# Kernel optimization log

Hardware: AMD Instinct MI355X
Metric: run time of the kernel (lower is better)

Reference implementation:

```python
import jax, jax.numpy as jnp
import numpy as np
import math

# ---- hyperparameters (from __init__) ----
S = 64.0
M = 0.45
EASY_MARGIN = False
ALPHA = 0.0
BETA = 0.0
EPS_OT = 0.1   # self.eps
NITER = 6      # self.niter
COS_M = math.cos(M)
SIN_M = math.sin(M)
TH = math.cos(math.pi - M)
MM = math.sin(math.pi - M) * M

# ---- shapes ----
B = 24
D_EMB = 512
N_CLASSES = 10000
C_CH = 256   # channels -> number of OT points per image
H = 14       # spatial -> point dim H*H = 196


def setup_inputs() -> dict:
    key = jax.random.key(0)
    k1, k2, k3, k4 = jax.random.split(key, 4)
    embeddings = jax.random.normal(k1, (B, D_EMB), dtype=jnp.float32)
    conv_features = jax.random.normal(k2, (B, C_CH, H, H), dtype=jnp.float32)
    label = jax.random.randint(k3, (B,), 0, 8)
    # nn.init.normal_(kernel, std=0.01)
    kernel = jax.random.normal(k4, (D_EMB, N_CLASSES), dtype=jnp.float32) * 0.01
    return {"embeddings": embeddings, "conv_features": conv_features,
            "kernel": kernel, "label": label, "epoch": 1}


def _cdist(x, y):
    # Euclidean pairwise distance via GEMM: x (n,d), y (m,d) -> (n,m)
    x2 = jnp.sum(x * x, axis=-1)[:, None]
    y2 = jnp.sum(y * y, axis=-1)[None, :]
    d2 = jnp.maximum(x2 + y2 - 2.0 * (x @ y.T), 0.0)
    return jnp.sqrt(d2 + 1e-12)


def _sinkhorn_dist(x, y):
    # Entropic OT distance <T, C> with uniform marginals, log-domain Sinkhorn.
    C = _cdist(x, y)                       # (n, m)
    n, m = C.shape
    log_mu = -jnp.log(jnp.float32(n))
    log_nu = -jnp.log(jnp.float32(m))
    f = jnp.zeros((n,), C.dtype)
    g = jnp.zeros((m,), C.dtype)
    for _ in range(NITER):  # fixed 6 iterations
        f = -EPS_OT * jax.nn.logsumexp((g[None, :] - C) / EPS_OT + log_nu, axis=1)
        g = -EPS_OT * jax.nn.logsumexp((f[:, None] - C) / EPS_OT + log_mu, axis=0)
    T = jnp.exp((f[:, None] + g[None, :] - C) / EPS_OT + log_mu + log_nu)
    return jnp.sum(T * C)


def reference(embeddings, conv_features, kernel, label, epoch):
    b = embeddings.shape[0]
    emb = embeddings / jnp.linalg.norm(embeddings, axis=1, keepdims=True)
    kn = kernel / jnp.linalg.norm(kernel, axis=0, keepdims=True)
    cos_theta = jnp.clip(emb @ kn, -1.0, 1.0)          # (B, n_classes)
    origin_cos = cos_theta

    rows = jnp.arange(b)
    tl = cos_theta[rows, label]                         # target logit (B,)
    sin_t = jnp.sqrt(jnp.maximum(1.0 - tl * tl, 0.0))
    ctm = tl * COS_M - sin_t * SIN_M
    if EASY_MARGIN:
        ftl = jnp.where(tl > 0.0, ctm, tl)
    else:
        ftl = jnp.where(tl > TH, ctm, tl - MM)
    cos_theta = cos_theta.at[rows, label].set(ftl)
    arcfaceloss = cos_theta * S

    # ---- triplet mining on embedding cosine similarities ----
    dists = emb @ emb.T                                 # (B, B) cosine sims
    eq = label[:, None] == label[None, :]               # (B, B) same-class mask
    # diff_low[a,p,n] = cos(a,n) - cos(a,p)
    diff = dists[:, None, :] - dists[:, :, None]        # (a, p, n)
    valid = eq[:, :, None] & (~eq)[:, None, :] & (diff > -ALPHA)
    n_cosine_pair = jnp.sum(valid)

    if epoch >= 0:
        feats = conv_features.reshape(b, conv_features.shape[1], -1)  # (B, C, H*H)
        # batched Sinkhorn distance for all (a,b) image pairs: (B, B)
        D = jax.vmap(lambda xa: jax.vmap(lambda xb: _sinkhorn_dist(xa, xb))(feats))(feats)
        dis = jnp.maximum(D[:, :, None] - D[:, None, :], -BETA)       # (a, p, n)
        hit = valid & (dis > 0.0)
        ot_pair = jnp.sum(hit)
        wass = jnp.sum(jnp.where(hit, dis, 0.0))
        wass_loss = jnp.where(wass > 0.0,
                              wass / jnp.maximum(ot_pair, 1).astype(wass.dtype),
                              jnp.zeros((), wass.dtype))
    else:
        ot_pair = jnp.zeros((), jnp.int32)
        wass_loss = jnp.zeros(())

    return (arcfaceloss, wass_loss, origin_cos * S, n_cosine_pair, ot_pair)
```

## Files before the change

kernel.cpp:

```cpp
#include <hip/hip_runtime.h>
#include <math.h>

#define B_SZ 24
#define D_EMBD 512
#define N_CLS 10000
#define CC 256
#define HH 196

#define S_SCALE 64.0f
#define COS_M 0.9004471023526769f
#define SIN_M 0.43496553411123023f
#define TH_C (-0.9004471023526769f)
#define MM_C 0.19573449035005357f
#define KSC 14.4269504088896f
#define C2E 0.0693147180559945f

typedef short bfrag8 __attribute__((ext_vector_type(8)));
typedef float facc4 __attribute__((ext_vector_type(4)));

#if __has_builtin(__builtin_amdgcn_exp2f)
#define EXP2F(x) __builtin_amdgcn_exp2f(x)
#else
#define EXP2F(x) exp2f(x)
#endif
#if __has_builtin(__builtin_amdgcn_logf)
#define LOG2F(x) __builtin_amdgcn_logf(x)
#else
#define LOG2F(x) __log2f(x)
#endif

__device__ inline unsigned short f2bf_rne(float x) {
    union { float f; unsigned u; } cv; cv.f = x;
    unsigned r = cv.u + 0x7FFFu + ((cv.u >> 16) & 1u);
    return (unsigned short)(r >> 16);
}
__device__ inline float bf2f(unsigned short h) {
    union { unsigned u; float f; } cv; cv.u = ((unsigned)h) << 16; return cv.f;
}

__global__ __launch_bounds__(1024) void k_pairs_all(const float* __restrict__ emb,
        const float* __restrict__ conv, float* __restrict__ dists,
        float* __restrict__ Dmat) {
    const int t = threadIdx.x;
    const int bid = blockIdx.x;

    if (bid >= 276) {
        int l = t & 63, w16 = t >> 6;
        if (bid == 276 && t < B_SZ) Dmat[t * B_SZ + t] = 0.f;
        int pid = (bid - 276) * 16 + w16;
        if (pid >= B_SZ * B_SZ) return;
        int i = pid / B_SZ, j = pid - (pid / B_SZ) * B_SZ;
        float sij = 0.f, sii = 0.f, sjj = 0.f;
        #pragma unroll
        for (int u = 0; u < 8; ++u) {
            float vi = emb[i*D_EMBD + u*64 + l];
            float vj = emb[j*D_EMBD + u*64 + l];
            sij = fmaf(vi, vj, sij); sii = fmaf(vi, vi, sii); sjj = fmaf(vj, vj, sjj);
        }
        #pragma unroll
        for (int o = 1; o < 64; o <<= 1) {
            sij += __shfl_xor(sij, o, 64);
            sii += __shfl_xor(sii, o, 64);
            sjj += __shfl_xor(sjj, o, 64);
        }
        if (l == 0) dists[pid] = sij * rsqrtf(sii * sjj);
        return;
    }

    __shared__ __align__(16) char smem[65536];
    unsigned short* Ah = (unsigned short*)smem;
    unsigned short* Al = Ah + 8192;
    unsigned short* Bh = Al + 8192;
    unsigned short* Bl = Bh + 8192;
    float* rowred = (float*)smem;
    float* colred = rowred + 1024;
    float* rm_l   = colred + 1024;
    float* z_l    = rm_l + 256;
    float* g_l    = z_l + 256;
    float* na_s   = g_l + 256;
    float* nb_s   = na_s + 256;
    float* wredF  = nb_s + 256;
    float* wredG  = wredF + 4;
    float* wredD  = wredG + 4;

    const int w = t >> 6;
    const int wr = w >> 2, wc = w & 3;
    const int q = (t >> 4) & 3, c0 = t & 15;
    const int R0 = wr * 64, C0 = wc * 64;

    int rem = bid, a = 0;
    while (rem >= 23 - a) { rem -= 23 - a; ++a; }
    int b = a + 1 + rem;
    const float* xa = conv + a*CC*HH;
    const float* xb = conv + b*CC*HH;

    const int sn = t >> 2;
    const int sch = t & 3;

    facc4 acc[4][4];
    #pragma unroll
    for (int i = 0; i < 4; ++i)
        #pragma unroll
        for (int j = 0; j < 4; ++j) acc[i][j] = (facc4){0.f, 0.f, 0.f, 0.f};

    float pa = 0.f, pb = 0.f;

    for (int ks = 0; ks < 224; ks += 32) {
        __syncthreads();
        #pragma unroll
        for (int p = 0; p < 2; ++p) {
            int k0 = ks + sch*8;
            const float* src = (p ? xb : xa) + sn*HH + k0;
            float v[8];
            if (k0 + 8 <= HH) {
                const float4* s4 = (const float4*)src;
                float4 u0 = s4[0], u1 = s4[1];
                v[0]=u0.x; v[1]=u0.y; v[2]=u0.z; v[3]=u0.w;
                v[4]=u1.x; v[5]=u1.y; v[6]=u1.z; v[7]=u1.w;
            } else {
                #pragma unroll
                for (int j = 0; j < 8; ++j) v[j] = (k0 + j < HH) ? src[j] : 0.f;
            }
            float ps = 0.f;
            union { unsigned short s[8]; bfrag8 v8; } uh, ul;
            #pragma unroll
            for (int j = 0; j < 8; ++j) {
                ps = fmaf(v[j], v[j], ps);
                unsigned short hb = f2bf_rne(v[j]);
                uh.s[j] = hb;
                ul.s[j] = f2bf_rne(v[j] - bf2f(hb));
            }
            if (p) pb += ps; else pa += ps;
            unsigned short* dh = (p ? Bh : Ah) + sn*32 + sch*8;
            unsigned short* dl = (p ? Bl : Al) + sn*32 + sch*8;
            *(bfrag8*)dh = uh.v8;
            *(bfrag8*)dl = ul.v8;
        }
        __syncthreads();
        bfrag8 bh4[4], bl4[4];
        #pragma unroll
        for (int tj = 0; tj < 4; ++tj) {
            int col = C0 + tj*16 + c0;
            bh4[tj] = *(const bfrag8*)(Bh + col*32 + q*8);
            bl4[tj] = *(const bfrag8*)(Bl + col*32 + q*8);
        }
        #pragma unroll
        for (int ti = 0; ti < 4; ++ti) {
            int row = R0 + ti*16 + c0;
            bfrag8 ah = *(const bfrag8*)(Ah + row*32 + q*8);
            bfrag8 al = *(const bfrag8*)(Al + row*32 + q*8);
            #pragma unroll
            for (int tj = 0; tj < 4; ++tj) {
                acc[ti][tj] = __builtin_amdgcn_mfma_f32_16x16x32_bf16(ah, bh4[tj], acc[ti][tj], 0, 0, 0);
                acc[ti][tj] = __builtin_amdgcn_mfma_f32_16x16x32_bf16(ah, bl4[tj], acc[ti][tj], 0, 0, 0);
                acc[ti][tj] = __builtin_amdgcn_mfma_f32_16x16x32_bf16(al, bh4[tj], acc[ti][tj], 0, 0, 0);
            }
        }
    }
    __syncthreads();

    pa += __shfl_xor(pa, 1, 64); pa += __shfl_xor(pa, 2, 64);
    pb += __shfl_xor(pb, 1, 64); pb += __shfl_xor(pb, 2, 64);
    if (sch == 0) { na_s[sn] = pa; nb_s[sn] = pb; }
    if (t < 256) g_l[t] = 0.f;
    if (t < 4) wredG[t] = 0.f;
    __syncthreads();

    facc4 E[4][4];
    {
        float nbv[4];
        #pragma unroll
        for (int tj = 0; tj < 4; ++tj) nbv[tj] = nb_s[C0 + tj*16 + c0];
        #pragma unroll
        for (int ti = 0; ti < 4; ++ti) {
            facc4 nav = *(const facc4*)&na_s[R0 + ti*16 + q*4];
            #pragma unroll
            for (int tj = 0; tj < 4; ++tj) {
                #pragma unroll
                for (int r = 0; r < 4; ++r) {
                    float d2 = fmaxf(nav[r] + nbv[tj] - 2.f*acc[ti][tj][r], 0.f);
                    E[ti][tj][r] = KSC * sqrtf(d2 + 1e-12f);
                }
            }
        }
    }

    const int istar = ((c0&1)<<3) | ((c0&2)<<1) | ((c0&4)>>1) | ((c0&8)>>3);
    const int rowstar = R0 + (istar>>2)*16 + q*4 + (istar&3);
    const int tjstar = ((q&1)<<1) | (q>>1);
    const int colstar = C0 + tjstar*16 + c0;

    {
        float v16[16];
        #pragma unroll
        for (int ti = 0; ti < 4; ++ti)
            #pragma unroll
            for (int r = 0; r < 4; ++r)
                v16[ti*4+r] = fminf(fminf(E[ti][0][r], E[ti][1][r]),
                                    fminf(E[ti][2][r], E[ti][3][r]));
        #pragma unroll
        for (int p = 0; p < 4; ++p) {
            const int m = 1 << p, hsz = 8 >> p;
            const bool hi = (c0 >> p) & 1;
            #pragma unroll
            for (int j = 0; j < hsz; ++j) {
                float mine = hi ? v16[j+hsz] : v16[j];
                float send = hi ? v16[j] : v16[j+hsz];
                v16[j] = fminf(mine, __shfl_xor(send, m, 64));
            }
        }
        rowred[wc*256 + rowstar] = v16[0];
    }
    __syncthreads();
    if (t < 256)
        rm_l[t] = fminf(fminf(rowred[t], rowred[256+t]), fminf(rowred[512+t], rowred[768+t]));
    __syncthreads();

    #pragma unroll
    for (int ti = 0; ti < 4; ++ti) {
        facc4 rmv = *(const facc4*)&rm_l[R0 + ti*16 + q*4];
        #pragma unroll
        for (int tj = 0; tj < 4; ++tj)
            #pragma unroll
            for (int r = 0; r < 4; ++r)
                E[ti][tj][r] = EXP2F(rmv[r] - E[ti][tj][r]);
    }

    #pragma unroll 1
    for (int it = 0; it < 6; ++it) {
        float Gmax = fmaxf(fmaxf(wredG[0], wredG[1]), fmaxf(wredG[2], wredG[3]));
        float P4[4];
        #pragma unroll
        for (int tj = 0; tj < 4; ++tj) P4[tj] = EXP2F(g_l[C0 + tj*16 + c0] - Gmax);
        float v16[16];
        #pragma unroll
        for (int ti = 0; ti < 4; ++ti)
            #pragma unroll
            for (int r = 0; r < 4; ++r) {
                float s = 0.f;
                #pragma unroll
                for (int tj = 0; tj < 4; ++tj) s = fmaf(E[ti][tj][r], P4[tj], s);
                v16[ti*4+r] = s;
            }
        #pragma unroll
        for (int p = 0; p < 4; ++p) {
            const int m = 1 << p, hsz = 8 >> p;
            const bool hi = (c0 >> p) & 1;
            #pragma unroll
            for (int j = 0; j < hsz; ++j) {
                float mine = hi ? v16[j+hsz] : v16[j];
                float send = hi ? v16[j] : v16[j+hsz];
                v16[j] = mine + __shfl_xor(send, m, 64);
            }
        }
        rowred[wc*256 + rowstar] = v16[0];
        __syncthreads();
        if (t < 256) {
            float s = rowred[t] + rowred[256+t] + rowred[512+t] + rowred[768+t];
            float z = 8.f - Gmax - LOG2F(s);
            z_l[t] = z;
            float m = z;
            #pragma unroll
            for (int o = 1; o < 64; o <<= 1) m = fmaxf(m, __shfl_xor(m, o, 64));
            if ((t & 63) == 0) wredF[t >> 6] = m;
        }
        __syncthreads();
        float M = fmaxf(fmaxf(wredF[0], wredF[1]), fmaxf(wredF[2], wredF[3]));
        float Q[16];
        #pragma unroll
        for (int ti = 0; ti < 4; ++ti) {
            facc4 zv = *(const facc4*)&z_l[R0 + ti*16 + q*4];
            #pragma unroll
            for (int r = 0; r < 4; ++r) Q[ti*4+r] = EXP2F(zv[r] - M);
        }
        float w4[4];
        #pragma unroll
        for (int tj = 0; tj < 4; ++tj) {
            float s = 0.f;
            #pragma unroll
            for (int ti = 0; ti < 4; ++ti)
                #pragma unroll
                for (int r = 0; r < 4; ++r) s = fmaf(E[ti][tj][r], Q[ti*4+r], s);
            w4[tj] = s;
        }
        #pragma unroll
        for (int p = 0; p < 2; ++p) {
            const int m = 16 << p, hsz = 2 >> p;
            const bool hi = (q >> p) & 1;
            #pragma unroll
            for (int j = 0; j < hsz; ++j) {
                float mine = hi ? w4[j+hsz] : w4[j];
                float send = hi ? w4[j] : w4[j+hsz];
                w4[j] = mine + __shfl_xor(send, m, 64);
            }
        }
        colred[wr*256 + colstar] = w4[0];
        __syncthreads();
        if (t < 256) {
            float s = colred[t] + colred[256+t] + colred[512+t] + colred[768+t];
            float G = 8.f - M - LOG2F(s);
            g_l[t] = G;
            float m = G;
            #pragma unroll
            for (int o = 1; o < 64; o <<= 1) m = fmaxf(m, __shfl_xor(m, o, 64));
            if ((t & 63) == 0) wredG[t >> 6] = m;
        }
        __syncthreads();
    }

    {
        float G4[4];
        #pragma unroll
        for (int tj = 0; tj < 4; ++tj) G4[tj] = g_l[C0 + tj*16 + c0] - 16.f;
        float d = 0.f;
        #pragma unroll
        for (int ti = 0; ti < 4; ++ti) {
            facc4 zv = *(const facc4*)&z_l[R0 + ti*16 + q*4];
            facc4 rmv = *(const facc4*)&rm_l[R0 + ti*16 + q*4];
            #pragma unroll
            for (int tj = 0; tj < 4; ++tj) {
                #pragma unroll
                for (int r = 0; r < 4; ++r) {
                    float e = fmaxf(E[ti][tj][r], 1e-45f);
                    float lE = LOG2F(e);
                    float ce = rmv[r] - lE;
                    d = fmaf(EXP2F(zv[r] + G4[tj] + lE), ce, d);
                }
            }
        }
        d *= C2E;
        #pragma unroll
        for (int o = 1; o < 64; o <<= 1) d += __shfl_xor(d, o, 64);
        if ((t & 63) == 0) wredD[w] = d;
        __syncthreads();
        if (t == 0) {
            float s = 0.f;
            #pragma unroll
            for (int i = 0; i < 16; ++i) s += wredD[i];
            Dmat[a*B_SZ + b] = s;
            Dmat[b*B_SZ + a] = s;
        }
    }
}

__global__ __launch_bounds__(256) void k_arc_fin(const float* __restrict__ emb,
        const float* __restrict__ kern, const int* __restrict__ label,
        const float* __restrict__ dists, const float* __restrict__ Dmat,
        float* __restrict__ out) {
    const int t = threadIdx.x;
    const int bid = blockIdx.x;

    if (bid == 313) {
        __shared__ float ds[576], Dm[576];
        __shared__ int lab[B_SZ];
        __shared__ float wls[4]; __shared__ int wnp[4], wot[4];
        for (int i = t; i < 576; i += 256) { ds[i] = dists[i]; Dm[i] = Dmat[i]; }
        if (t < B_SZ) lab[t] = label[t];
        __syncthreads();
        int np = 0, ot = 0; float wsum = 0.f;
        for (int idx = t; idx < 24*24*24; idx += 256) {
            int a2 = idx / 576;
            int rest = idx - a2*576;
            int p2 = rest / 24;
            int n2 = rest - p2*24;
            int la = lab[a2];
            if (la == lab[p2] && la != lab[n2]) {
                float diff = ds[a2*24 + n2] - ds[a2*24 + p2];
                if (diff > 0.f) {
                    ++np;
                    float dd = Dm[a2*24 + p2] - Dm[a2*24 + n2];
                    if (dd > 0.f) { ++ot; wsum += dd; }
                }
            }
        }
        #pragma unroll
        for (int o = 1; o < 64; o <<= 1) {
            np += __shfl_xor(np, o, 64);
            ot += __shfl_xor(ot, o, 64);
            wsum += __shfl_xor(wsum, o, 64);
        }
        int w = t >> 6;
        if ((t & 63) == 0) { wnp[w] = np; wot[w] = ot; wls[w] = wsum; }
        __syncthreads();
        if (t == 0) {
            int tnp = wnp[0]+wnp[1]+wnp[2]+wnp[3];
            int tot = wot[0]+wot[1]+wot[2]+wot[3];
            float tws = wls[0]+wls[1]+wls[2]+wls[3];
            int den = tot > 1 ? tot : 1;
            float wl = (tws > 0.f) ? tws / (float)den : 0.f;
            out[240000] = wl;
            out[480001] = (float)tnp;
            out[480002] = (float)tot;
        }
        return;
    }

    __shared__ __align__(16) float es[B_SZ*D_EMBD];
    __shared__ float inv_s[B_SZ];
    __shared__ int lab_s[B_SZ];
    float* part = es;
    float* resb = es + 6400;

    {
        const float4* s4 = (const float4*)emb;
        float4* d4 = (float4*)es;
        for (int i = t; i < (B_SZ*D_EMBD)/4; i += 256) d4[i] = s4[i];
    }
    if (t < B_SZ) lab_s[t] = label[t];
    __syncthreads();
    {
        int l = t & 63, w = t >> 6;
        for (int r = w; r < B_SZ; r += 4) {
            float s = 0.f;
            #pragma unroll
            for (int u = 0; u < 8; ++u) { float v = es[r*D_EMBD + u*64 + l]; s = fmaf(v, v, s); }
            #pragma unroll
            for (int o = 1; o < 64; o <<= 1) s += __shfl_xor(s, o, 64);
            if (l == 0) inv_s[r] = rsqrtf(s);
        }
    }
    __syncthreads();

    const int cc = t & 31, kc = t >> 5;
    int c = bid*32 + cc;
    int cL = c < N_CLS ? c : N_CLS - 1;
    float acc[B_SZ];
    #pragma unroll
    for (int r = 0; r < B_SZ; ++r) acc[r] = 0.f;
    float cn = 0.f;
    const int k0 = kc*64;
    for (int u = 0; u < 16; ++u) {
        int kb = k0 + u*4;
        float kv0 = kern[(kb+0)*N_CLS + cL];
        float kv1 = kern[(kb+1)*N_CLS + cL];
        float kv2 = kern[(kb+2)*N_CLS + cL];
        float kv3 = kern[(kb+3)*N_CLS + cL];
        cn = fmaf(kv0,kv0,cn); cn = fmaf(kv1,kv1,cn);
        cn = fmaf(kv2,kv2,cn); cn = fmaf(kv3,kv3,cn);
        #pragma unroll
        for (int r = 0; r < B_SZ; ++r) {
            const float4 e = *(const float4*)&es[r*D_EMBD + kb];
            acc[r] = fmaf(e.x, kv0, acc[r]);
            acc[r] = fmaf(e.y, kv1, acc[r]);
            acc[r] = fmaf(e.z, kv2, acc[r]);
            acc[r] = fmaf(e.w, kv3, acc[r]);
        }
    }
    __syncthreads();
    #pragma unroll
    for (int r = 0; r < B_SZ; ++r) part[kc*800 + cc*25 + r] = acc[r];
    part[kc*800 + cc*25 + 24] = cn;
    __syncthreads();
    for (int j = t; j < 800; j += 256) {
        float s = 0.f;
        #pragma unroll
        for (int kk = 0; kk < 8; ++kk) s += part[kk*800 + j];
        resb[j] = s;
    }
    __syncthreads();
    for (int o = t; o < 768; o += 256) {
        int r = o >> 5, c2 = o & 31;
        int col = bid*32 + c2;
        if (col >= N_CLS) continue;
        float dot = resb[c2*25 + r];
        float invk = rsqrtf(resb[c2*25 + 24]);
        float cosv = fminf(fmaxf(dot * inv_s[r] * invk, -1.f), 1.f);
        float oc = cosv * S_SCALE;
        float af = oc;
        if (lab_s[r] == col) {
            float tl = cosv;
            float sint = sqrtf(fmaxf(1.f - tl*tl, 0.f));
            float ctm = tl*COS_M - sint*SIN_M;
            float ftl = (tl > TH_C) ? ctm : (tl - MM_C);
            af = ftl * S_SCALE;
        }
        out[r*N_CLS + col] = af;
        out[240001 + r*N_CLS + col] = oc;
    }
}

extern "C" void kernel_launch(void* const* d_in, const int* in_sizes, int n_in,
                              void* d_out, int out_size, void* d_ws, size_t ws_size,
                              hipStream_t stream) {
    (void)in_sizes; (void)n_in; (void)out_size; (void)ws_size;
    const float* emb  = (const float*)d_in[0];
    const float* conv = (const float*)d_in[1];
    const float* kern = (const float*)d_in[2];
    const int*   lab  = (const int*)d_in[3];
    float* out = (float*)d_out;
    float* ws  = (float*)d_ws;
    float* dists = ws;
    float* Dmat  = ws + 576;

    k_pairs_all<<<312, 1024, 0, stream>>>(emb, conv, dists, Dmat);
    k_arc_fin<<<314, 256, 0, stream>>>(emb, kern, lab, dists, Dmat, out);
}
```

Measured before the change: 204.8 us.

## Fuse ArcFace GEMM into pairs kernel and split final reduction into tiny kernel

Moves the ArcFace cosine GEMM out of the second kernel and into extra blocks of the main Sinkhorn pairs kernel, so it runs concurrently with the OT work instead of after it. The GEMM is remapped to 1024-thread blocks covering 256 classes each, with 4-way k-splits reduced through shuffles instead of shared memory. The triplet/final reduction becomes a separate single-block kernel. The cost is fewer, larger ArcFace blocks with 24 accumulators per thread plus higher shared memory per block, which may hurt occupancy or the balance of the tail.

```diff
diff --git a/kernel.cpp b/kernel.cpp
--- a/kernel.cpp
+++ b/kernel.cpp
@@ -6,6 +6,10 @@
 #define N_CLS 10000
 #define CC 256
 #define HH 196
+
+#define NPAIR 276
+#define NARC 40
+#define NGRAM 36
 
 #define S_SCALE 64.0f
 #define COS_M 0.9004471023526769f
@@ -38,36 +42,119 @@
     union { unsigned u; float f; } cv; cv.u = ((unsigned)h) << 16; return cv.f;
 }
 
-__global__ __launch_bounds__(1024) void k_pairs_all(const float* __restrict__ emb,
-        const float* __restrict__ conv, float* __restrict__ dists,
-        float* __restrict__ Dmat) {
+__global__ __launch_bounds__(1024) void k_fused(const float* __restrict__ emb,
+        const float* __restrict__ conv, const float* __restrict__ kern,
+        const int* __restrict__ label, float* __restrict__ dists,
+        float* __restrict__ Dmat, float* __restrict__ out) {
     const int t = threadIdx.x;
     const int bid = blockIdx.x;
 
-    if (bid >= 276) {
-        int l = t & 63, w16 = t >> 6;
-        if (bid == 276 && t < B_SZ) Dmat[t * B_SZ + t] = 0.f;
-        int pid = (bid - 276) * 16 + w16;
-        if (pid >= B_SZ * B_SZ) return;
-        int i = pid / B_SZ, j = pid - (pid / B_SZ) * B_SZ;
-        float sij = 0.f, sii = 0.f, sjj = 0.f;
-        #pragma unroll
-        for (int u = 0; u < 8; ++u) {
-            float vi = emb[i*D_EMBD + u*64 + l];
-            float vj = emb[j*D_EMBD + u*64 + l];
-            sij = fmaf(vi, vj, sij); sii = fmaf(vi, vi, sii); sjj = fmaf(vj, vj, sjj);
-        }
-        #pragma unroll
-        for (int o = 1; o < 64; o <<= 1) {
-            sij += __shfl_xor(sij, o, 64);
-            sii += __shfl_xor(sii, o, 64);
-            sjj += __shfl_xor(sjj, o, 64);
-        }
-        if (l == 0) dists[pid] = sij * rsqrtf(sii * sjj);
+    __shared__ __align__(16) char smem[65536];
+
+    if (bid >= NPAIR) {
+        const int sb = bid - NPAIR;
+        if (sb >= NARC) {
+            const int gid = sb - NARC;
+            int l = t & 63, w16 = t >> 6;
+            if (gid == 0 && t < B_SZ) Dmat[t * B_SZ + t] = 0.f;
+            int pid = gid * 16 + w16;
+            if (pid >= B_SZ * B_SZ) return;
+            int i = pid / B_SZ, j = pid - (pid / B_SZ) * B_SZ;
+            float sij = 0.f, sii = 0.f, sjj = 0.f;
+            #pragma unroll
+            for (int u = 0; u < 8; ++u) {
+                float vi = emb[i*D_EMBD + u*64 + l];
+                float vj = emb[j*D_EMBD + u*64 + l];
+                sij = fmaf(vi, vj, sij); sii = fmaf(vi, vi, sii); sjj = fmaf(vj, vj, sjj);
+            }
+            #pragma unroll
+            for (int o = 1; o < 64; o <<= 1) {
+                sij += __shfl_xor(sij, o, 64);
+                sii += __shfl_xor(sii, o, 64);
+                sjj += __shfl_xor(sjj, o, 64);
+            }
+            if (l == 0) dists[pid] = sij * rsqrtf(sii * sjj);
+            return;
+        }
+
+        float* es = (float*)smem;
+        float* inv_s = es + B_SZ * D_EMBD;
+        int* lab_s = (int*)(inv_s + B_SZ);
+
+        {
+            const float4* s4 = (const float4*)emb;
+            float4* d4 = (float4*)es;
+            #pragma unroll
+            for (int i = 0; i < 3; ++i) d4[i*1024 + t] = s4[i*1024 + t];
+        }
+        if (t < B_SZ) lab_s[t] = label[t];
+        __syncthreads();
+        {
+            int l = t & 63, w = t >> 6;
+            for (int r = w; r < B_SZ; r += 16) {
+                float s = 0.f;
+                #pragma unroll
+                for (int u = 0; u < 8; ++u) { float v = es[r*D_EMBD + u*64 + l]; s = fmaf(v, v, s); }
+                #pragma unroll
+                for (int o = 1; o < 64; o <<= 1) s += __shfl_xor(s, o, 64);
+                if (l == 0) inv_s[r] = rsqrtf(s);
+            }
+        }
+        __syncthreads();
+
+        const int cc = t >> 2, kc = t & 3;
+        const int col = sb * 256 + cc;
+        const int cL = col < N_CLS ? col : N_CLS - 1;
+        float acc[B_SZ];
+        #pragma unroll
+        for (int r = 0; r < B_SZ; ++r) acc[r] = 0.f;
+        float cn = 0.f;
+        const int kb0 = kc << 7;
+        for (int u = 0; u < 32; ++u) {
+            const int um = (u + kc) & 31;
+            const int kb = kb0 + (um << 2);
+            float kv0 = kern[(kb+0)*N_CLS + cL];
+            float kv1 = kern[(kb+1)*N_CLS + cL];
+            float kv2 = kern[(kb+2)*N_CLS + cL];
+            float kv3 = kern[(kb+3)*N_CLS + cL];
+            cn = fmaf(kv0,kv0,cn); cn = fmaf(kv1,kv1,cn);
+            cn = fmaf(kv2,kv2,cn); cn = fmaf(kv3,kv3,cn);
+            #pragma unroll
+            for (int r = 0; r < B_SZ; ++r) {
+                const float4 e = *(const float4*)&es[r*D_EMBD + kb];
+                acc[r] = fmaf(e.x, kv0, acc[r]);
+                acc[r] = fmaf(e.y, kv1, acc[r]);
+                acc[r] = fmaf(e.z, kv2, acc[r]);
+                acc[r] = fmaf(e.w, kv3, acc[r]);
+            }
+        }
+        cn += __shfl_xor(cn, 1, 64); cn += __shfl_xor(cn, 2, 64);
+        #pragma unroll
+        for (int r = 0; r < B_SZ; ++r) {
+            acc[r] += __shfl_xor(acc[r], 1, 64);
+            acc[r] += __shfl_xor(acc[r], 2, 64);
+        }
+        if (kc == 0 && col < N_CLS) {
+            const float invk = rsqrtf(cn);
+            #pragma unroll
+            for (int r = 0; r < B_SZ; ++r) {
+                float cosv = fminf(fmaxf(acc[r] * inv_s[r] * invk, -1.f), 1.f);
+                float oc = cosv * S_SCALE;
+                float af = oc;
+                if (lab_s[r] == col) {
+                    float tl = cosv;
+                    float sint = sqrtf(fmaxf(1.f - tl*tl, 0.f));
+                    float ctm = tl*COS_M - sint*SIN_M;
+                    float ftl = (tl > TH_C) ? ctm : (tl - MM_C);
+                    af = ftl * S_SCALE;
+                }
+                out[r*N_CLS + col] = af;
+                out[240001 + r*N_CLS + col] = oc;
+            }
+        }
         return;
     }
 
-    __shared__ __align__(16) char smem[65536];
     unsigned short* Ah = (unsigned short*)smem;
     unsigned short* Al = Ah + 8192;
     unsigned short* Bh = Al + 8192;
@@ -343,139 +430,50 @@
     }
 }
 
-__global__ __launch_bounds__(256) void k_arc_fin(const float* __restrict__ emb,
-        const float* __restrict__ kern, const int* __restrict__ label,
+__global__ __launch_bounds__(256) void k_fin(const int* __restrict__ label,
         const float* __restrict__ dists, const float* __restrict__ Dmat,
         float* __restrict__ out) {
     const int t = threadIdx.x;
-    const int bid = blockIdx.x;
-
-    if (bid == 313) {
-        __shared__ float ds[576], Dm[576];
-        __shared__ int lab[B_SZ];
-        __shared__ float wls[4]; __shared__ int wnp[4], wot[4];
-        for (int i = t; i < 576; i += 256) { ds[i] = dists[i]; Dm[i] = Dmat[i]; }
-        if (t < B_SZ) lab[t] = label[t];
-        __syncthreads();
-        int np = 0, ot = 0; float wsum = 0.f;
-        for (int idx = t; idx < 24*24*24; idx += 256) {
-            int a2 = idx / 576;
-            int rest = idx - a2*576;
-            int p2 = rest / 24;
-            int n2 = rest - p2*24;
-            int la = lab[a2];
-            if (la == lab[p2] && la != lab[n2]) {
-                float diff = ds[a2*24 + n2] - ds[a2*24 + p2];
-                if (diff > 0.f) {
-                    ++np;
-                    float dd = Dm[a2*24 + p2] - Dm[a2*24 + n2];
-                    if (dd > 0.f) { ++ot; wsum += dd; }
-                }
-            }
-        }
-        #pragma unroll
-        for (int o = 1; o < 64; o <<= 1) {
-            np += __shfl_xor(np, o, 64);
-            ot += __shfl_xor(ot, o, 64);
-            wsum += __shfl_xor(wsum, o, 64);
-        }
-        int w = t >> 6;
-        if ((t & 63) == 0) { wnp[w] = np; wot[w] = ot; wls[w] = wsum; }
-        __syncthreads();
-        if (t == 0) {
-            int tnp = wnp[0]+wnp[1]+wnp[2]+wnp[3];
-            int tot = wot[0]+wot[1]+wot[2]+wot[3];
-            float tws = wls[0]+wls[1]+wls[2]+wls[3];
-            int den = tot > 1 ? tot : 1;
-            float wl = (tws > 0.f) ? tws / (float)den : 0.f;
-            out[240000] = wl;
-            out[480001] = (float)tnp;
-            out[480002] = (float)tot;
-        }
-        return;
-    }
-
-    __shared__ __align__(16) float es[B_SZ*D_EMBD];
-    __shared__ float inv_s[B_SZ];
-    __shared__ int lab_s[B_SZ];
-    float* part = es;
-    float* resb = es + 6400;
-
-    {
-        const float4* s4 = (const float4*)emb;
-        float4* d4 = (float4*)es;
-        for (int i = t; i < (B_SZ*D_EMBD)/4; i += 256) d4[i] = s4[i];
-    }
-    if (t < B_SZ) lab_s[t] = label[t];
-    __syncthreads();
-    {
-        int l = t & 63, w = t >> 6;
-        for (int r = w; r < B_SZ; r += 4) {
-            float s = 0.f;
-            #pragma unroll
-            for (int u = 0; u < 8; ++u) { float v = es[r*D_EMBD + u*64 + l]; s = fmaf(v, v, s); }
-            #pragma unroll
-            for (int o = 1; o < 64; o <<= 1) s += __shfl_xor(s, o, 64);
-            if (l == 0) inv_s[r] = rsqrtf(s);
-        }
-    }
-    __syncthreads();
-
-    const int cc = t & 31, kc = t >> 5;
-    int c = bid*32 + cc;
-    int cL = c < N_CLS ? c : N_CLS - 1;
-    float acc[B_SZ];
+    __shared__ float ds[576], Dm[576];
+    __shared__ int lab[B_SZ];
+    __shared__ float wls[4]; __shared__ int wnp[4], wot[4];
+    for (int i = t; i < 576; i += 256) { ds[i] = dists[i]; Dm[i] = Dmat[i]; }
+    if (t < B_SZ) lab[t] = label[t];
+    __syncthreads();
+    int np = 0, ot = 0; float wsum = 0.f;
+    for (int idx = t; idx < 24*24*24; idx += 256) {
+        int a2 = idx / 576;
+        int rest = idx - a2*576;
+        int p2 = rest / 24;
+        int n2 = rest - p2*24;
+        int la = lab[a2];
+        if (la == lab[p2] && la != lab[n2]) {
+            float diff = ds[a2*24 + n2] - ds[a2*24 + p2];
+            if (diff > 0.f) {
+                ++np;
+                float dd = Dm[a2*24 + p2] - Dm[a2*24 + n2];
+                if (dd > 0.f) { ++ot; wsum += dd; }
+            }
+        }
+    }
     #pragma unroll
-    for (int r = 0; r < B_SZ; ++r) acc[r] = 0.f;
-    float cn = 0.f;
-    const int k0 = kc*64;
-    for (int u = 0; u < 16; ++u) {
-        int kb = k0 + u*4;
-        float kv0 = kern[(kb+0)*N_CLS + cL];
-        float kv1 = kern[(kb+1)*N_CLS + cL];
-        float kv2 = kern[(kb+2)*N_CLS + cL];
-        float kv3 = kern[(kb+3)*N_CLS + cL];
-        cn = fmaf(kv0,kv0,cn); cn = fmaf(kv1,kv1,cn);
-        cn = fmaf(kv2,kv2,cn); cn = fmaf(kv3,kv3,cn);
-        #pragma unroll
-        for (int r = 0; r < B_SZ; ++r) {
-            const float4 e = *(const float4*)&es[r*D_EMBD + kb];
-            acc[r] = fmaf(e.x, kv0, acc[r]);
-            acc[r] = fmaf(e.y, kv1, acc[r]);
-            acc[r] = fmaf(e.z, kv2, acc[r]);
-            acc[r] = fmaf(e.w, kv3, acc[r]);
-        }
-    }
-    __syncthreads();
-    #pragma unroll
-    for (int r = 0; r < B_SZ; ++r) part[kc*800 + cc*25 + r] = acc[r];
-    part[kc*800 + cc*25 + 24] = cn;
-    __syncthreads();
-    for (int j = t; j < 800; j += 256) {
-        float s = 0.f;
-        #pragma unroll
-        for (int kk = 0; kk < 8; ++kk) s += part[kk*800 + j];
-        resb[j] = s;
-    }
-    __syncthreads();
-    for (int o = t; o < 768; o += 256) {
-        int r = o >> 5, c2 = o & 31;
-        int col = bid*32 + c2;
-        if (col >= N_CLS) continue;
-        float dot = resb[c2*25 + r];
-        float invk = rsqrtf(resb[c2*25 + 24]);
-        float cosv = fminf(fmaxf(dot * inv_s[r] * invk, -1.f), 1.f);
-        float oc = cosv * S_SCALE;
-        float af = oc;
-        if (lab_s[r] == col) {
-            float tl = cosv;
-            float sint = sqrtf(fmaxf(1.f - tl*tl, 0.f));
-            float ctm = tl*COS_M - sint*SIN_M;
-            float ftl = (tl > TH_C) ? ctm : (tl - MM_C);
-            af = ftl * S_SCALE;
-        }
-        out[r*N_CLS + col] = af;
-        out[240001 + r*N_CLS + col] = oc;
+    for (int o = 1; o < 64; o <<= 1) {
+        np += __shfl_xor(np, o, 64);
+        ot += __shfl_xor(ot, o, 64);
+        wsum += __shfl_xor(wsum, o, 64);
+    }
+    int w = t >> 6;
+    if ((t & 63) == 0) { wnp[w] = np; wot[w] = ot; wls[w] = wsum; }
+    __syncthreads();
+    if (t == 0) {
+        int tnp = wnp[0]+wnp[1]+wnp[2]+wnp[3];
+        int tot = wot[0]+wot[1]+wot[2]+wot[3];
+        float tws = wls[0]+wls[1]+wls[2]+wls[3];
+        int den = tot > 1 ? tot : 1;
+        float wl = (tws > 0.f) ? tws / (float)den : 0.f;
+        out[240000] = wl;
+        out[480001] = (float)tnp;
+        out[480002] = (float)tot;
     }
 }
 
@@ -492,6 +490,6 @@
     float* dists = ws;
     float* Dmat  = ws + 576;
 
-    k_pairs_all<<<312, 1024, 0, stream>>>(emb, conv, dists, Dmat);
-    k_arc_fin<<<314, 256, 0, stream>>>(emb, kern, lab, dists, Dmat, out);
+    k_fused<<<NPAIR + NARC + NGRAM, 1024, 0, stream>>>(emb, conv, kern, lab, dists, Dmat, out);
+    k_fin<<<1, 256, 0, stream>>>(lab, dists, Dmat, out);
 }
```

After: 198.6 us, median of 2. 3.0% less time.
